# Performance work log

Measured on AMD Instinct MI355X. Metric: run time of the kernel, lower is better.

## Reference

```python
import jax, jax.numpy as jnp
import numpy as np

N = 50000      # nodes
E = 800000     # edges (before self-loops)
FEAT = 128     # input feature dim F
HID = 32       # per-head hidden H
HEADS = 8      # n_head
C = 40         # classes
NEG_SLOPE = 0.2


def setup_inputs() -> dict:
    key = jax.random.key(0)
    ks = jax.random.split(key, 12)
    x = jax.random.normal(ks[0], (N, FEAT), jnp.float32)
    edge_index = jax.random.randint(ks[1], (2, E), 0, N, jnp.int32)
    s1 = 1.0 / np.sqrt(FEAT)
    s2 = 1.0 / np.sqrt(HEADS * HID)
    W1 = jax.random.normal(ks[2], (FEAT, HEADS * HID), jnp.float32) * s1
    a1_src = jax.random.normal(ks[3], (HEADS, HID), jnp.float32) * s2
    a1_dst = jax.random.normal(ks[4], (HEADS, HID), jnp.float32) * s2
    b1 = jnp.zeros((HEADS * HID,), jnp.float32)
    W2 = jax.random.normal(ks[5], (HEADS * HID, HEADS * HID), jnp.float32) * s2
    a2_src = jax.random.normal(ks[6], (HEADS, HID), jnp.float32) * s2
    a2_dst = jax.random.normal(ks[7], (HEADS, HID), jnp.float32) * s2
    b2 = jnp.zeros((HEADS * HID,), jnp.float32)
    Wc = jax.random.normal(ks[8], (HEADS * HID, C), jnp.float32) * s2
    bc = jnp.zeros((C,), jnp.float32)
    return {"x": x, "edge_index": edge_index,
            "W1": W1, "a1_src": a1_src, "a1_dst": a1_dst, "b1": b1,
            "W2": W2, "a2_src": a2_src, "a2_dst": a2_dst, "b2": b2,
            "Wc": Wc, "bc": bc}


def gat_conv(x, src, dst, W, a_src, a_dst, b):
    # x: [N, F_in] -> per-head features [N, heads, H]
    n = x.shape[0]
    xh = (x @ W).reshape(n, HEADS, HID)
    alpha_s = jnp.einsum('nhd,hd->nh', xh, a_src)   # [N, heads]
    alpha_d = jnp.einsum('nhd,hd->nh', xh, a_dst)   # [N, heads]
    e = alpha_s[src] + alpha_d[dst]                  # [E, heads]
    e = jnp.where(e > 0, e, NEG_SLOPE * e)           # LeakyReLU(0.2)
    # softmax over incoming edges grouped by destination node
    emax = jax.ops.segment_max(e, dst, num_segments=n)
    ex = jnp.exp(e - emax[dst])
    denom = jax.ops.segment_sum(ex, dst, num_segments=n)
    alpha = ex / denom[dst]                          # [E, heads]
    msg = xh[src] * alpha[:, :, None]                # [E, heads, H]
    out = jax.ops.segment_sum(msg, dst, num_segments=n)
    return out.reshape(n, HEADS * HID) + b


def reference(x, edge_index, W1, a1_src, a1_dst, b1, W2, a2_src, a2_dst, b2, Wc, bc):
    # PyG GATConv adds self-loops by default
    loops = jnp.arange(N, dtype=edge_index.dtype)
    ei = jnp.concatenate([edge_index, jnp.stack([loops, loops])], axis=1)
    src, dst = ei[0], ei[1]
    h = gat_conv(x, src, dst, W1, a1_src, a1_dst, b1)
    h = jax.nn.relu(h)
    h = gat_conv(h, src, dst, W2, a2_src, a2_dst, b2)
    h = jax.nn.relu(h)
    return h @ Wc + bc
```

## Files before the change

### kernel.cpp

```cpp
#include <hip/hip_runtime.h>
#include <math.h>

#define NNODES 50000
#define NEDGES 800000
#define NTOT   850000
#define NHEAD  8
#define HDIM   32
#define HHD    256
#define NCLS   40
#define NEG_SLOPE 0.2f

typedef _Float16 half4 __attribute__((ext_vector_type(4)));
typedef _Float16 half8 __attribute__((ext_vector_type(8)));
typedef float f32x16 __attribute__((ext_vector_type(16)));
typedef unsigned short u16;


__global__ void k_init_counts(int* __restrict__ counts) {
    int i = blockIdx.x * 256 + threadIdx.x;
    if (i < NNODES) counts[i] = 1;
}

__global__ void k_count(const int* __restrict__ ei, int* __restrict__ counts) {
    int i = blockIdx.x * 256 + threadIdx.x;
    if (i < NEDGES) atomicAdd(&counts[ei[NEDGES + i]], 1);
}

__global__ __launch_bounds__(256) void k_scan1(const int* __restrict__ counts,
                                               int* __restrict__ partial,
                                               int* __restrict__ bsums) {
    __shared__ int lds[256];
    int t = threadIdx.x;
    int i = blockIdx.x * 256 + t;
    int v = (i < NNODES) ? counts[i] : 0;
    lds[t] = v;
    __syncthreads();
    for (int off = 1; off < 256; off <<= 1) {
        int add = (t >= off) ? lds[t - off] : 0;
        __syncthreads();
        lds[t] += add;
        __syncthreads();
    }
    if (i < NNODES) partial[i] = lds[t] - v;
    if (t == 255) bsums[blockIdx.x] = lds[255];
}

__global__ __launch_bounds__(256) void k_scan2(const int* __restrict__ bsums,
                                               int* __restrict__ boff, int nb) {
    __shared__ int lds[256];
    int t = threadIdx.x;
    int v = (t < nb) ? bsums[t] : 0;
    lds[t] = v;
    __syncthreads();
    for (int off = 1; off < 256; off <<= 1) {
        int add = (t >= off) ? lds[t - off] : 0;
        __syncthreads();
        lds[t] += add;
        __syncthreads();
    }
    if (t < nb) boff[t] = lds[t] - v;
}

__global__ void k_scan3(int* __restrict__ row_ptr, const int* __restrict__ boff,
                        int* __restrict__ cursor) {
    int i = blockIdx.x * 256 + threadIdx.x;
    if (i < NNODES) {
        int r = row_ptr[i] + boff[blockIdx.x];
        row_ptr[i] = r;
        cursor[i] = r;
    }
    if (i == 0) row_ptr[NNODES] = NTOT;
}

__global__ void k_scatter(const int* __restrict__ ei, int* __restrict__ cursor,
                          int* __restrict__ esrc) {
    int i = blockIdx.x * 256 + threadIdx.x;
    if (i < NEDGES) {
        int s = ei[i];
        int d = ei[NEDGES + i];
        int pos = atomicAdd(&cursor[d], 1);
        esrc[pos] = s;
    } else if (i < NTOT) {
        int n = i - NEDGES;
        int pos = atomicAdd(&cursor[n], 1);
        esrc[pos] = n;
    }
}

__global__ void k_prep_all(const float* __restrict__ W1, const float* __restrict__ W2,
                           const float* __restrict__ Wc,
                           _Float16* __restrict__ w1t, _Float16* __restrict__ w2t,
                           _Float16* __restrict__ wct) {
    int gid = blockIdx.x * 256 + threadIdx.x;
    if (gid >= 256 * 64) return;
    int frag = gid >> 6, l = gid & 63;
    const float* W; _Float16* Wt; int K, Nc, fkn, fbase;
    if (frag < 64)       { W = W1; Wt = w1t; K = 128; Nc = 256; fkn = 8;  fbase = 0; }
    else if (frag < 192) { W = W2; Wt = w2t; K = 256; Nc = 256; fkn = 16; fbase = 64; }
    else                 { W = Wc; Wt = wct; K = 256; Nc = 40;  fkn = 16; fbase = 192; }
    int f = frag - fbase;
    int fn = f / fkn, fk = f - fn * fkn;
    int n = fn * 32 + (l & 31);
    int k = fk * 16 + ((l >> 5) << 3);
    half8 v;
    #pragma unroll
    for (int j = 0; j < 8; ++j)
        v[j] = (n < Nc) ? (_Float16)W[(size_t)(k + j) * Nc + n] : (_Float16)0.f;
    *reinterpret_cast<half8*>(Wt + ((size_t)f * 64 + l) * 8) = v;
}

#define TBM 64
#define TBN 128
#define TBK 32
#define APAD 34
#define LDCT 132

template <typename AT, int K, int MODE>
__global__ __launch_bounds__(256) void k_mfma_gemm(
    const AT* __restrict__ A,
    const _Float16* __restrict__ Wt,
    _Float16* __restrict__ Ch,
    float* __restrict__ Cf,
    const float* __restrict__ bias,
    const float* __restrict__ a_src,
    const float* __restrict__ a_dst,
    float* __restrict__ alpha_s,
    float* __restrict__ alpha_d,
    int M, int ldc)
{
    constexpr bool A_IS_F32 = sizeof(AT) == 4;
    constexpr int SMEM_ELEMS = (MODE == 0) ? TBM * LDCT : TBM * APAD;
    __shared__ _Float16 smem[SMEM_ELEMS];
    int t = threadIdx.x;
    int lane = t & 63;
    int wid = t >> 6;
    int wr = wid >> 1, wc = wid & 1;
    int rowBase = blockIdx.y * TBM;
    int colBase = blockIdx.x * TBN;

    int arow = t >> 2;
    int akoff = (t & 3) * 8;
    bool arow_ok = (rowBase + arow) < M;
    const AT* aptr = A + (size_t)(rowBase + arow) * K + akoff;

    constexpr int FKN = K >> 4;
    size_t bbase[2];
    #pragma unroll
    for (int ct = 0; ct < 2; ++ct) {
        int fn = blockIdx.x * 4 + wc * 2 + ct;
        bbase[ct] = ((size_t)fn * FKN) * 512 + (size_t)lane * 8;
    }

    f32x16 acc[2];
    #pragma unroll
    for (int j = 0; j < 2; ++j)
        #pragma unroll
        for (int r = 0; r < 16; ++r) acc[j][r] = 0.f;

    float4 aregf[2];
    half8  aregh;
    auto load_a = [&](const AT* ap) {
        if constexpr (A_IS_F32) {
            #pragma unroll
            for (int i = 0; i < 2; ++i)
                aregf[i] = arow_ok ? *reinterpret_cast<const float4*>((const float*)ap + i * 4)
                                   : float4{0.f, 0.f, 0.f, 0.f};
        } else {
            aregh = arow_ok ? *reinterpret_cast<const half8*>((const _Float16*)ap)
                            : half8{0, 0, 0, 0, 0, 0, 0, 0};
        }
    };
    load_a(aptr);

    half8 bf0[2], bf1[2];
    #pragma unroll
    for (int ct = 0; ct < 2; ++ct) {
        bf0[ct] = *reinterpret_cast<const half8*>(Wt + bbase[ct]);
        bf1[ct] = *reinterpret_cast<const half8*>(Wt + bbase[ct] + 512);
    }

    #pragma unroll
    for (int k0 = 0; k0 < K; k0 += TBK) {
        half8 hv;
        if constexpr (A_IS_F32) {
            hv[0] = (_Float16)aregf[0].x; hv[1] = (_Float16)aregf[0].y;
            hv[2] = (_Float16)aregf[0].z; hv[3] = (_Float16)aregf[0].w;
            hv[4] = (_Float16)aregf[1].x; hv[5] = (_Float16)aregf[1].y;
            hv[6] = (_Float16)aregf[1].z; hv[7] = (_Float16)aregf[1].w;
        } else {
            hv = aregh;
        }
        *reinterpret_cast<half8*>(&smem[arow * APAD + akoff]) = hv;
        __syncthreads();
        if (k0 + TBK < K) load_a(aptr + k0 + TBK);
        half8 bn0[2], bn1[2];
        if (k0 + TBK < K) {
            #pragma unroll
            for (int ct = 0; ct < 2; ++ct) {
                size_t nb = bbase[ct] + (size_t)((k0 >> 4) + 2) * 512;
                bn0[ct] = *reinterpret_cast<const half8*>(Wt + nb);
                bn1[ct] = *reinterpret_cast<const half8*>(Wt + nb + 512);
            }
        }
        #pragma unroll
        for (int sub = 0; sub < 2; ++sub) {
            int kfo = sub * 16 + (lane >> 5) * 8;
            half8 ah = *reinterpret_cast<const half8*>(
                &smem[(wr * 32 + (lane & 31)) * APAD + kfo]);
            #pragma unroll
            for (int ct = 0; ct < 2; ++ct)
                acc[ct] = __builtin_amdgcn_mfma_f32_32x32x16_f16(
                    ah, (sub == 0) ? bf0[ct] : bf1[ct], acc[ct], 0, 0, 0);
        }
        if (k0 + TBK < K) {
            #pragma unroll
            for (int ct = 0; ct < 2; ++ct) { bf0[ct] = bn0[ct]; bf1[ct] = bn1[ct]; }
        }
        __syncthreads();
    }

    if constexpr (MODE == 0) {
        #pragma unroll
        for (int ct = 0; ct < 2; ++ct) {
            int lcol = wc * 64 + ct * 32 + (lane & 31);
            #pragma unroll
            for (int r = 0; r < 16; ++r) {
                int lrow = wr * 32 + (r & 3) + 8 * (r >> 2) + 4 * (lane >> 5);
                smem[lrow * LDCT + lcol] = (_Float16)acc[ct][r];
            }
        }
        __syncthreads();
        #pragma unroll
        for (int pass = 0; pass < 4; ++pass) {
            int idx = t + pass * 256;
            int lrow = idx >> 4;
            int cchunk = (idx & 15) * 8;
            int grow = rowBase + lrow;
            if (grow < M) {
                half8 v = *reinterpret_cast<const half8*>(&smem[lrow * LDCT + cchunk]);
                *reinterpret_cast<half8*>(Ch + (size_t)grow * ldc + colBase + cchunk) = v;
            }
        }
        {
            int lrow = t >> 2, hoff = t & 3;
            int grow = rowBase + lrow;
            if (grow < M) {
                int h = blockIdx.x * 4 + hoff;
                const float* as4 = a_src + h * HDIM;
                const float* ad4 = a_dst + h * HDIM;
                float ss = 0.f, sd = 0.f;
                #pragma unroll
                for (int j = 0; j < HDIM; ++j) {
                    float v = (float)smem[lrow * LDCT + hoff * 32 + j];
                    ss += v * as4[j];
                    sd += v * ad4[j];
                }
                alpha_s[grow * NHEAD + h] = ss;
                alpha_d[grow * NHEAD + h] = sd;
            }
        }
    } else {
        #pragma unroll
        for (int ct = 0; ct < 2; ++ct) {
            int col = colBase + wc * 64 + ct * 32 + (lane & 31);
            #pragma unroll
            for (int r = 0; r < 16; ++r) {
                int row = rowBase + wr * 32 + (r & 3) + 8 * (r >> 2) + 4 * (lane >> 5);
                if (row < M && col < NCLS)
                    Cf[(size_t)row * ldc + col] = acc[ct][r] + bias[col];
            }
        }
    }
}

__global__ __launch_bounds__(256) void k_agg(const _Float16* __restrict__ xh,
                                             const float* __restrict__ alpha_s,
                                             const float* __restrict__ alpha_d,
                                             const int* __restrict__ row_ptr,
                                             const int* __restrict__ esrc,
                                             const float* __restrict__ bias,
                                             _Float16* __restrict__ out) {
    int wave = blockIdx.x * 4 + (threadIdx.x >> 6);
    int node = wave * 2 + ((threadIdx.x & 63) >> 5);
    if (node >= NNODES) return;
    int l = threadIdx.x & 31;
    int h = l >> 2;
    int beg = row_ptr[node], end = row_ptr[node + 1];
    float ad = alpha_d[node * NHEAD + h];
    float acc[8] = {};
    float ssum = 0.f;
    int i = beg;
    for (; i + 3 < end; i += 4) {
        int s0 = esrc[i], s1 = esrc[i + 1], s2 = esrc[i + 2], s3 = esrc[i + 3];
        float e0 = alpha_s[s0 * NHEAD + h] + ad;
        float e1 = alpha_s[s1 * NHEAD + h] + ad;
        float e2 = alpha_s[s2 * NHEAD + h] + ad;
        float e3 = alpha_s[s3 * NHEAD + h] + ad;
        half8 v0 = *reinterpret_cast<const half8*>(xh + (size_t)s0 * HHD + l * 8);
        half8 v1 = *reinterpret_cast<const half8*>(xh + (size_t)s1 * HHD + l * 8);
        half8 v2 = *reinterpret_cast<const half8*>(xh + (size_t)s2 * HHD + l * 8);
        half8 v3 = *reinterpret_cast<const half8*>(xh + (size_t)s3 * HHD + l * 8);
        e0 = (e0 > 0.f) ? e0 : NEG_SLOPE * e0;
        e1 = (e1 > 0.f) ? e1 : NEG_SLOPE * e1;
        e2 = (e2 > 0.f) ? e2 : NEG_SLOPE * e2;
        e3 = (e3 > 0.f) ? e3 : NEG_SLOPE * e3;
        float p0 = __expf(e0), p1 = __expf(e1), p2 = __expf(e2), p3 = __expf(e3);
        ssum += (p0 + p1) + (p2 + p3);
        #pragma unroll
        for (int d = 0; d < 8; ++d)
            acc[d] += p0 * (float)v0[d] + p1 * (float)v1[d] +
                      p2 * (float)v2[d] + p3 * (float)v3[d];
    }
    for (; i < end; ++i) {
        int s0 = esrc[i];
        float e0 = alpha_s[s0 * NHEAD + h] + ad;
        half8 v0 = *reinterpret_cast<const half8*>(xh + (size_t)s0 * HHD + l * 8);
        e0 = (e0 > 0.f) ? e0 : NEG_SLOPE * e0;
        float p0 = __expf(e0);
        ssum += p0;
        #pragma unroll
        for (int d = 0; d < 8; ++d)
            acc[d] += p0 * (float)v0[d];
    }
    float inv = 1.f / ssum;
    float4 b0 = *reinterpret_cast<const float4*>(bias + l * 8);
    float4 b1 = *reinterpret_cast<const float4*>(bias + l * 8 + 4);
    float bb[8] = {b0.x, b0.y, b0.z, b0.w, b1.x, b1.y, b1.z, b1.w};
    half8 r;
    #pragma unroll
    for (int d = 0; d < 8; ++d)
        r[d] = (_Float16)fmaxf(acc[d] * inv + bb[d], 0.f);
    *reinterpret_cast<half8*>(out + (size_t)node * HHD + l * 8) = r;
}


extern "C" void kernel_launch(void* const* d_in, const int* in_sizes, int n_in,
                              void* d_out, int out_size, void* d_ws, size_t ws_size,
                              hipStream_t stream) {
    const float* x   = (const float*)d_in[0];
    const int*   ei  = (const int*)  d_in[1];
    const float* W1  = (const float*)d_in[2];
    const float* a1s = (const float*)d_in[3];
    const float* a1d = (const float*)d_in[4];
    const float* b1  = (const float*)d_in[5];
    const float* W2  = (const float*)d_in[6];
    const float* a2s = (const float*)d_in[7];
    const float* a2d = (const float*)d_in[8];
    const float* b2  = (const float*)d_in[9];
    const float* Wc  = (const float*)d_in[10];
    const float* bc  = (const float*)d_in[11];
    float* out = (float*)d_out;

    char* ws = (char*)d_ws;
    size_t off = 0;
    auto alloc = [&](size_t bytes) -> void* {
        void* p = ws + off;
        off += (bytes + 255) & ~(size_t)255;
        return p;
    };
    _Float16* xh_h   = (_Float16*)alloc((size_t)NNODES * HHD * 2);
    _Float16* hbuf_h = (_Float16*)alloc((size_t)NNODES * HHD * 2);
    float* as_   = (float*)alloc((size_t)NNODES * NHEAD * 4);
    float* ad_   = (float*)alloc((size_t)NNODES * NHEAD * 4);
    int* counts  = (int*)alloc((size_t)NNODES * 4);
    int* row_ptr = (int*)alloc((size_t)(NNODES + 1) * 4);
    int* cursor  = (int*)alloc((size_t)NNODES * 4);
    int* esrc    = (int*)alloc((size_t)NTOT * 4);
    int* bsums   = (int*)alloc(256 * 4);
    int* boff    = (int*)alloc(256 * 4);
    _Float16* w1t = (_Float16*)alloc((size_t)64 * 64 * 8 * 2);
    _Float16* w2t = (_Float16*)alloc((size_t)128 * 64 * 8 * 2);
    _Float16* wct = (_Float16*)alloc((size_t)64 * 64 * 8 * 2);
    (void)ws_size; (void)in_sizes; (void)n_in; (void)out_size;

    int gn = (NNODES + 255) / 256;
    int ge = (NEDGES + 255) / 256;
    int gt = (NTOT + 255) / 256;

    k_init_counts<<<gn, 256, 0, stream>>>(counts);
    k_count<<<ge, 256, 0, stream>>>(ei, counts);
    k_scan1<<<gn, 256, 0, stream>>>(counts, row_ptr, bsums);
    k_scan2<<<1, 256, 0, stream>>>(bsums, boff, gn);
    k_scan3<<<gn, 256, 0, stream>>>(row_ptr, boff, cursor);
    k_scatter<<<gt, 256, 0, stream>>>(ei, cursor, esrc);

    k_prep_all<<<64, 256, 0, stream>>>(W1, W2, Wc, w1t, w2t, wct);

    dim3 gHid(HHD / TBN, (NNODES + TBM - 1) / TBM);
    dim3 gCls(1, (NNODES + TBM - 1) / TBM);
    int gagg = NNODES / 8;

    k_mfma_gemm<float, 128, 0><<<gHid, 256, 0, stream>>>(
        x, w1t, xh_h, nullptr, nullptr, a1s, a1d, as_, ad_, NNODES, HHD);
    k_agg<<<gagg, 256, 0, stream>>>(xh_h, as_, ad_, row_ptr, esrc, b1, hbuf_h);

    k_mfma_gemm<_Float16, 256, 0><<<gHid, 256, 0, stream>>>(
        hbuf_h, w2t, xh_h, nullptr, nullptr, a2s, a2d, as_, ad_, NNODES, HHD);
    k_agg<<<gagg, 256, 0, stream>>>(xh_h, as_, ad_, row_ptr, esrc, b2, hbuf_h);

    k_mfma_gemm<_Float16, 256, 1><<<gCls, 256, 0, stream>>>(
        hbuf_h, wct, nullptr, out, bc, nullptr, nullptr, nullptr, nullptr,
        NNODES, NCLS);
}
```

Measured before the change: 311.7 us.

## Stage full-K A tile in LDS once and replace count-init kernel with memset

The MFMA GEMM no longer walks K in 32-wide chunks with two barriers per chunk. It now loads the whole K extent of the A tile (converted to fp16) into LDS up front, syncs once, then runs all MFMA k-steps, reading B fragments straight from global memory. The aim is to cut barrier and pipeline overhead and to put more loads in flight. The cost is a larger LDS footprint (about 33KB for K=256), which may reduce occupancy, and the removal of explicit B register prefetching. Separately, the counts-init kernel becomes a hipMemsetAsync, with the self-loop +1 folded into the first scan pass.

```diff
diff --git a/kernel.cpp b/kernel.cpp
--- a/kernel.cpp
+++ b/kernel.cpp
@@ -16,11 +16,6 @@
 typedef unsigned short u16;
 
 
-__global__ void k_init_counts(int* __restrict__ counts) {
-    int i = blockIdx.x * 256 + threadIdx.x;
-    if (i < NNODES) counts[i] = 1;
-}
-
 __global__ void k_count(const int* __restrict__ ei, int* __restrict__ counts) {
     int i = blockIdx.x * 256 + threadIdx.x;
     if (i < NEDGES) atomicAdd(&counts[ei[NEDGES + i]], 1);
@@ -32,7 +27,7 @@
     __shared__ int lds[256];
     int t = threadIdx.x;
     int i = blockIdx.x * 256 + t;
-    int v = (i < NNODES) ? counts[i] : 0;
+    int v = (i < NNODES) ? counts[i] + 1 : 0;
     lds[t] = v;
     __syncthreads();
     for (int off = 1; off < 256; off <<= 1) {
@@ -111,8 +106,6 @@
 
 #define TBM 64
 #define TBN 128
-#define TBK 32
-#define APAD 34
 #define LDCT 132
 
 template <typename AT, int K, int MODE>
@@ -129,7 +122,10 @@
     int M, int ldc)
 {
     constexpr bool A_IS_F32 = sizeof(AT) == 4;
-    constexpr int SMEM_ELEMS = (MODE == 0) ? TBM * LDCT : TBM * APAD;
+    constexpr int APADK = K + 2;
+    constexpr int A_ELEMS = TBM * APADK;
+    constexpr int CT_ELEMS = (MODE == 0) ? TBM * LDCT : 0;
+    constexpr int SMEM_ELEMS = (A_ELEMS > CT_ELEMS) ? A_ELEMS : CT_ELEMS;
     __shared__ _Float16 smem[SMEM_ELEMS];
     int t = threadIdx.x;
     int lane = t & 63;
@@ -139,9 +135,9 @@
     int colBase = blockIdx.x * TBN;
 
     int arow = t >> 2;
-    int akoff = (t & 3) * 8;
+    int acoff = (t & 3) * (K / 4);
     bool arow_ok = (rowBase + arow) < M;
-    const AT* aptr = A + (size_t)(rowBase + arow) * K + akoff;
+    const AT* aptr = A + (size_t)(rowBase + arow) * K + acoff;
 
     constexpr int FKN = K >> 4;
     size_t bbase[2];
@@ -157,67 +153,40 @@
         #pragma unroll
         for (int r = 0; r < 16; ++r) acc[j][r] = 0.f;
 
-    float4 aregf[2];
-    half8  aregh;
-    auto load_a = [&](const AT* ap) {
-        if constexpr (A_IS_F32) {
-            #pragma unroll
-            for (int i = 0; i < 2; ++i)
-                aregf[i] = arow_ok ? *reinterpret_cast<const float4*>((const float*)ap + i * 4)
-                                   : float4{0.f, 0.f, 0.f, 0.f};
-        } else {
-            aregh = arow_ok ? *reinterpret_cast<const half8*>((const _Float16*)ap)
-                            : half8{0, 0, 0, 0, 0, 0, 0, 0};
-        }
-    };
-    load_a(aptr);
-
-    half8 bf0[2], bf1[2];
-    #pragma unroll
-    for (int ct = 0; ct < 2; ++ct) {
-        bf0[ct] = *reinterpret_cast<const half8*>(Wt + bbase[ct]);
-        bf1[ct] = *reinterpret_cast<const half8*>(Wt + bbase[ct] + 512);
-    }
-
-    #pragma unroll
-    for (int k0 = 0; k0 < K; k0 += TBK) {
+    #pragma unroll
+    for (int c = 0; c < K / 32; ++c) {
         half8 hv;
         if constexpr (A_IS_F32) {
-            hv[0] = (_Float16)aregf[0].x; hv[1] = (_Float16)aregf[0].y;
-            hv[2] = (_Float16)aregf[0].z; hv[3] = (_Float16)aregf[0].w;
-            hv[4] = (_Float16)aregf[1].x; hv[5] = (_Float16)aregf[1].y;
-            hv[6] = (_Float16)aregf[1].z; hv[7] = (_Float16)aregf[1].w;
+            float4 v0 = {0.f, 0.f, 0.f, 0.f}, v1 = {0.f, 0.f, 0.f, 0.f};
+            if (arow_ok) {
+                v0 = *reinterpret_cast<const float4*>((const float*)aptr + c * 8);
+                v1 = *reinterpret_cast<const float4*>((const float*)aptr + c * 8 + 4);
+            }
+            hv[0] = (_Float16)v0.x; hv[1] = (_Float16)v0.y;
+            hv[2] = (_Float16)v0.z; hv[3] = (_Float16)v0.w;
+            hv[4] = (_Float16)v1.x; hv[5] = (_Float16)v1.y;
+            hv[6] = (_Float16)v1.z; hv[7] = (_Float16)v1.w;
         } else {
-            hv = aregh;
-        }
-        *reinterpret_cast<half8*>(&smem[arow * APAD + akoff]) = hv;
-        __syncthreads();
-        if (k0 + TBK < K) load_a(aptr + k0 + TBK);
-        half8 bn0[2], bn1[2];
-        if (k0 + TBK < K) {
-            #pragma unroll
-            for (int ct = 0; ct < 2; ++ct) {
-                size_t nb = bbase[ct] + (size_t)((k0 >> 4) + 2) * 512;
-                bn0[ct] = *reinterpret_cast<const half8*>(Wt + nb);
-                bn1[ct] = *reinterpret_cast<const half8*>(Wt + nb + 512);
-            }
-        }
-        #pragma unroll
-        for (int sub = 0; sub < 2; ++sub) {
-            int kfo = sub * 16 + (lane >> 5) * 8;
-            half8 ah = *reinterpret_cast<const half8*>(
-                &smem[(wr * 32 + (lane & 31)) * APAD + kfo]);
-            #pragma unroll
-            for (int ct = 0; ct < 2; ++ct)
-                acc[ct] = __builtin_amdgcn_mfma_f32_32x32x16_f16(
-                    ah, (sub == 0) ? bf0[ct] : bf1[ct], acc[ct], 0, 0, 0);
-        }
-        if (k0 + TBK < K) {
-            #pragma unroll
-            for (int ct = 0; ct < 2; ++ct) { bf0[ct] = bn0[ct]; bf1[ct] = bn1[ct]; }
-        }
-        __syncthreads();
-    }
+            hv = arow_ok ? *reinterpret_cast<const half8*>((const _Float16*)aptr + c * 8)
+                         : half8{0, 0, 0, 0, 0, 0, 0, 0};
+        }
+        *reinterpret_cast<half8*>(&smem[arow * APADK + acoff + c * 8]) = hv;
+    }
+    __syncthreads();
+
+    #pragma unroll
+    for (int fk = 0; fk < FKN; ++fk) {
+        int kfo = fk * 16 + (lane >> 5) * 8;
+        half8 ah = *reinterpret_cast<const half8*>(
+            &smem[(wr * 32 + (lane & 31)) * APADK + kfo]);
+        #pragma unroll
+        for (int ct = 0; ct < 2; ++ct) {
+            half8 bh = *reinterpret_cast<const half8*>(
+                Wt + bbase[ct] + (size_t)fk * 512);
+            acc[ct] = __builtin_amdgcn_mfma_f32_32x32x16_f16(ah, bh, acc[ct], 0, 0, 0);
+        }
+    }
+    __syncthreads();
 
     if constexpr (MODE == 0) {
         #pragma unroll
@@ -377,7 +346,7 @@
     int ge = (NEDGES + 255) / 256;
     int gt = (NTOT + 255) / 256;
 
-    k_init_counts<<<gn, 256, 0, stream>>>(counts);
+    hipMemsetAsync(counts, 0, (size_t)NNODES * 4, stream);
     k_count<<<ge, 256, 0, stream>>>(ei, counts);
     k_scan1<<<gn, 256, 0, stream>>>(counts, row_ptr, bsums);
     k_scan2<<<1, 256, 0, stream>>>(bsums, boff, gn);
```

After: 322.7 us. 1.04x slower.
